# Kernel tuning notes

Measured on AMD Instinct MI355X. Metric: run time of the kernel, lower is better.

The kernel has to match this reference:

```python
import jax, jax.numpy as jnp
import numpy as np

EMBED = 1024
HEADS = 16
HEAD_DIM = EMBED // HEADS
NEG = -1e20


def setup_inputs() -> dict:
    key = jax.random.key(0)
    ks = jax.random.split(key, 12)
    N, S, E = 2, 2048, EMBED
    w = lambda k: (jax.random.normal(k, (E, E), dtype=jnp.float32) * 0.02)
    b = lambda k: (jax.random.normal(k, (E,), dtype=jnp.float32) * 0.02)
    return {
        "values": jax.random.normal(ks[0], (N, S, E), dtype=jnp.float32),
        "keys": jax.random.normal(ks[1], (N, S, E), dtype=jnp.float32),
        "query": jax.random.normal(ks[2], (N, S, E), dtype=jnp.float32),
        "mask": jnp.ones((N, S), dtype=jnp.int32),
        "Wv": w(ks[3]), "bv": b(ks[4]),
        "Wk": w(ks[5]), "bk": b(ks[6]),
        "Wq": w(ks[7]), "bq": b(ks[8]),
        "Wo": w(ks[9]), "bo": b(ks[10]),
    }


def reference(values, keys, query, mask, Wv, bv, Wk, bk, Wq, bq, Wo, bo):
    N, S, E = query.shape
    # torch nn.Linear: x @ W.T + b
    v = (values @ Wv.T + bv).reshape(N, S, HEADS, HEAD_DIM)
    k = (keys @ Wk.T + bk).reshape(N, S, HEADS, HEAD_DIM)
    q = (query @ Wq.T + bq).reshape(N, S, HEADS, HEAD_DIM)
    # full [N,H,Q,K] score matrix, as in the original einsum
    energy = jnp.einsum('nqhd,nkhd->nhqk', q, k)
    # 2D mask with mismatched dims triggers causal tril path in the original
    causal = jnp.tril(jnp.ones((S, S), dtype=bool))  # [Q,K]
    energy = jnp.where(causal[None, None, :, :], energy, NEG)
    # NOTE: original scales by sqrt(embed_size), not sqrt(head_dim)
    attn = jax.nn.softmax(energy / jnp.sqrt(jnp.float32(E)), axis=3)
    out = jnp.einsum('nhqk,nkhd->nqhd', attn, v).reshape(N, S, E)
    return out @ Wo.T + bo
```

## Files before the change

kernel.cpp:

```cpp
#include <hip/hip_runtime.h>

typedef __bf16 bf16;
typedef __bf16 bf16x8 __attribute__((ext_vector_type(8)));
typedef float floatx4 __attribute__((ext_vector_type(4)));

#define GLOAD_LDS16(gp, lp) \
  __builtin_amdgcn_global_load_lds( \
      (const __attribute__((address_space(1))) void*)(gp), \
      (__attribute__((address_space(3))) void*)(lp), 16, 0, 0)

__global__ __launch_bounds__(256) void cvt_all_kernel(
    const float* __restrict__ v, const float* __restrict__ k, const float* __restrict__ q,
    const float* __restrict__ wv, const float* __restrict__ wk,
    const float* __restrict__ wq, const float* __restrict__ wo,
    bf16* __restrict__ xv, bf16* __restrict__ xk, bf16* __restrict__ xq,
    bf16* __restrict__ bwv, bf16* __restrict__ bwk, bf16* __restrict__ bwq,
    bf16* __restrict__ bwo) {
  const int i = blockIdx.x * 256 + threadIdx.x;
  const int A4 = 1 << 20;
  const float* src; bf16* dst; int off;
  if (i < A4)            { src = v; dst = xv; off = i; }
  else if (i < 2 * A4)   { src = k; dst = xk; off = i - A4; }
  else if (i < 3 * A4)   { src = q; dst = xq; off = i - 2 * A4; }
  else {
    int j = i - 3 * A4; int r = j >> 18; off = j & ((1 << 18) - 1);
    src = (r == 0) ? wv : (r == 1) ? wk : (r == 2) ? wq : wo;
    dst = (r == 0) ? bwv : (r == 1) ? bwk : (r == 2) ? bwq : bwo;
  }
  float4 x = reinterpret_cast<const float4*>(src)[off];
  union { bf16 b[4]; short4 s; } u;
  u.b[0] = (bf16)x.x; u.b[1] = (bf16)x.y; u.b[2] = (bf16)x.z; u.b[3] = (bf16)x.w;
  reinterpret_cast<short4*>(dst)[off] = u.s;
}

template <bool OUTF32>
__device__ __forceinline__ void gemm_body(
    const bf16* __restrict__ A, const bf16* __restrict__ B,
    const float* __restrict__ bias, void* __restrict__ Cout) {
  constexpr int K = 1024, N = 1024;
  __shared__ __align__(16) bf16 As[128 * 32];
  __shared__ __align__(16) bf16 Bs[128 * 32];
  const int tid = threadIdx.x;
  const int lane = tid & 63;
  const int wave = tid >> 6;
  const int quad = lane >> 4;
  const int l16 = lane & 15;
  const int wm = (wave >> 1) * 64;
  const int wn = (wave & 1) * 64;
  const int am0 = blockIdx.y * 128;
  const int bn0 = blockIdx.x * 128;
  const int srow = lane >> 2;
  const int scol = (lane & 3) * 8;

  floatx4 acc[4][4] = {};

  for (int k0 = 0; k0 < K; k0 += 32) {
    __syncthreads();
#pragma unroll
    for (int j = 0; j < 2; j++) {
      const int chunk = wave * 2 + j;
      const int row = chunk * 16 + srow;
      GLOAD_LDS16(A + (size_t)(am0 + row) * K + k0 + scol, As + chunk * 512);
      GLOAD_LDS16(B + (size_t)(bn0 + row) * K + k0 + scol, Bs + chunk * 512);
    }
    __syncthreads();

    bf16x8 af[4], bfv[4];
#pragma unroll
    for (int mi = 0; mi < 4; mi++)
      af[mi] = *reinterpret_cast<const bf16x8*>(&As[(wm + mi * 16 + l16) * 32 + quad * 8]);
#pragma unroll
    for (int ni = 0; ni < 4; ni++)
      bfv[ni] = *reinterpret_cast<const bf16x8*>(&Bs[(wn + ni * 16 + l16) * 32 + quad * 8]);
#pragma unroll
    for (int mi = 0; mi < 4; mi++)
#pragma unroll
      for (int ni = 0; ni < 4; ni++)
        acc[mi][ni] = __builtin_amdgcn_mfma_f32_16x16x32_bf16(af[mi], bfv[ni], acc[mi][ni], 0, 0, 0);
  }

#pragma unroll
  for (int mi = 0; mi < 4; mi++) {
#pragma unroll
    for (int ni = 0; ni < 4; ni++) {
      const int col = bn0 + wn + ni * 16 + l16;
      const float bb = bias[col];
      const int row = am0 + wm + mi * 16 + quad * 4;
#pragma unroll
      for (int r = 0; r < 4; r++) {
        const float vv = acc[mi][ni][r] + bb;
        if constexpr (OUTF32)
          reinterpret_cast<float*>(Cout)[(size_t)(row + r) * N + col] = vv;
        else
          reinterpret_cast<bf16*>(Cout)[(size_t)(row + r) * N + col] = (bf16)vv;
      }
    }
  }
}

__global__ __launch_bounds__(256) void gemm_qkv(
    const bf16* __restrict__ A0, const bf16* __restrict__ B0, const float* __restrict__ c0, bf16* __restrict__ C0,
    const bf16* __restrict__ A1, const bf16* __restrict__ B1, const float* __restrict__ c1, bf16* __restrict__ C1,
    const bf16* __restrict__ A2, const bf16* __restrict__ B2, const float* __restrict__ c2, bf16* __restrict__ C2) {
  const bf16 *A, *B; const float* bias; bf16* C;
  if (blockIdx.z == 0)      { A = A0; B = B0; bias = c0; C = C0; }
  else if (blockIdx.z == 1) { A = A1; B = B1; bias = c1; C = C1; }
  else                      { A = A2; B = B2; bias = c2; C = C2; }
  gemm_body<false>(A, B, bias, C);
}

__global__ __launch_bounds__(256) void gemm_out(
    const bf16* __restrict__ A, const bf16* __restrict__ B,
    const float* __restrict__ bias, float* __restrict__ C) {
  gemm_body<true>(A, B, bias, C);
}

__global__ __launch_bounds__(256) void vtrans_kernel(
    const bf16* __restrict__ Vp, bf16* __restrict__ Vt) {
  __shared__ __align__(16) bf16 T[64 * 72];
  const int st = blockIdx.x;
  const int nh = blockIdx.y;
  const int n = nh >> 4, h = nh & 15;
  const int tid = threadIdx.x;
  {
    int c = tid;
#pragma unroll
    for (int it = 0; it < 2; it++, c += 256) {
      int r = c >> 3, col = (c & 7) * 8;
      *reinterpret_cast<int4*>(&T[r * 72 + col]) =
          *reinterpret_cast<const int4*>(Vp + ((size_t)(n * 2048 + st * 64 + r)) * 1024 + h * 64 + col);
    }
  }
  __syncthreads();
  {
    int c = tid;
#pragma unroll
    for (int it = 0; it < 2; it++, c += 256) {
      int d = c >> 3, sc = (c & 7) * 8;
      union { bf16 b[8]; int4 v; } tmp;
#pragma unroll
      for (int j = 0; j < 8; j++) tmp.b[j] = T[(sc + j) * 72 + d];
      *reinterpret_cast<int4*>(Vt + ((size_t)(nh * 64 + d)) * 2048 + st * 64 + sc) = tmp.v;
    }
  }
}

#define S_LEN 2048
#define EMB 1024
#define QT 128
#define KTILE 64
#define PSTR 72
#define SCALE2 (0.03125f * 1.44269504f)

__global__ __launch_bounds__(256) void attn_kernel(
    const bf16* __restrict__ Q, const bf16* __restrict__ K,
    const bf16* __restrict__ Vt, bf16* __restrict__ O) {
  __shared__ __align__(16) bf16 Ps[QT * PSTR];

  const int tid = threadIdx.x;
  const int lane = tid & 63;
  const int wave = tid >> 6;
  const int quad = lane >> 4;
  const int l16 = lane & 15;
  const int wq = wave * 32;

  const int id = blockIdx.x;
  const int p = id & 255;
  const int half = id >> 8;
  const int qtl = p & 7;
  const int qt = half ? (15 - qtl) : qtl;
  const int nh = p >> 3;
  const int n = nh >> 4;
  const int h = nh & 15;
  const int q0 = qt * QT;

  bf16x8 aq[2][2];
  {
    const bf16* Qb = Q + ((size_t)(n * S_LEN + q0 + wq + l16)) * EMB + h * 64 + quad * 8;
#pragma unroll
    for (int mi = 0; mi < 2; mi++)
#pragma unroll
      for (int kc = 0; kc < 2; kc++)
        aq[mi][kc] = *reinterpret_cast<const bf16x8*>(Qb + mi * 16 * EMB + kc * 32);
  }

  float l_part[2][4] = {};
  floatx4 o_acc[2][4] = {};

  const bf16* Kb = K + ((size_t)(n * S_LEN + l16)) * EMB + h * 64 + quad * 8;
  const bf16* Vb = Vt + (size_t)(nh * 64 + l16) * S_LEN + quad * 8;

  const int ktiles = 2 * qt + 2;
  for (int kt = 0; kt < ktiles; kt++) {
    const int k0 = kt * KTILE;

    floatx4 s_acc[2][4] = {};
#pragma unroll
    for (int kc = 0; kc < 2; kc++) {
      bf16x8 bk[4];
#pragma unroll
      for (int ni = 0; ni < 4; ni++)
        bk[ni] = *reinterpret_cast<const bf16x8*>(Kb + (size_t)(k0 + ni * 16) * EMB + kc * 32);
#pragma unroll
      for (int mi = 0; mi < 2; mi++)
#pragma unroll
        for (int ni = 0; ni < 4; ni++)
          s_acc[mi][ni] = __builtin_amdgcn_mfma_f32_16x16x32_bf16(aq[mi][kc], bk[ni], s_acc[mi][ni], 0, 0, 0);
    }

    const bool needMask = (k0 + KTILE - 1) > (q0 + wq);
#pragma unroll
    for (int mi = 0; mi < 2; mi++) {
#pragma unroll
      for (int ni = 0; ni < 4; ni++) {
        const int cg = k0 + ni * 16 + l16;
#pragma unroll
        for (int r = 0; r < 4; r++) {
          const int rg = q0 + wq + mi * 16 + quad * 4 + r;
          float pr = __builtin_amdgcn_exp2f(s_acc[mi][ni][r] * SCALE2);
          if (needMask) pr = (cg <= rg) ? pr : 0.f;
          s_acc[mi][ni][r] = pr;
          l_part[mi][r] += pr;
        }
      }
    }

#pragma unroll
    for (int mi = 0; mi < 2; mi++) {
#pragma unroll
      for (int ni = 0; ni < 4; ni++) {
        const int cl = ni * 2 + (l16 >> 3);
        const int pc = (cl ^ quad) * 8 + (l16 & 7);
#pragma unroll
        for (int r = 0; r < 4; r++)
          Ps[(wq + mi * 16 + quad * 4 + r) * PSTR + pc] = (bf16)s_acc[mi][ni][r];
      }
    }

#pragma unroll
    for (int kc = 0; kc < 2; kc++) {
      bf16x8 ap[2], bv[4];
      const int pc = ((kc * 4 + quad) ^ (l16 >> 2)) * 8;
#pragma unroll
      for (int mi = 0; mi < 2; mi++)
        ap[mi] = *reinterpret_cast<const bf16x8*>(&Ps[(wq + mi * 16 + l16) * PSTR + pc]);
#pragma unroll
      for (int di = 0; di < 4; di++)
        bv[di] = *reinterpret_cast<const bf16x8*>(Vb + (size_t)(di * 16) * S_LEN + k0 + kc * 32);
#pragma unroll
      for (int mi = 0; mi < 2; mi++)
#pragma unroll
        for (int di = 0; di < 4; di++)
          o_acc[mi][di] = __builtin_amdgcn_mfma_f32_16x16x32_bf16(ap[mi], bv[di], o_acc[mi][di], 0, 0, 0);
    }
  }

#pragma unroll
  for (int mi = 0; mi < 2; mi++)
#pragma unroll
    for (int r = 0; r < 4; r++) {
      float s = l_part[mi][r];
#pragma unroll
      for (int off = 1; off < 16; off <<= 1) s += __shfl_xor(s, off);
      l_part[mi][r] = 1.0f / s;
    }

  bf16* Op = O + ((size_t)(n * S_LEN + q0 + wq)) * EMB + h * 64;
#pragma unroll
  for (int mi = 0; mi < 2; mi++) {
#pragma unroll
    for (int r = 0; r < 4; r++) {
      const float inv = l_part[mi][r];
      bf16* orow = Op + (size_t)(mi * 16 + quad * 4 + r) * EMB;
#pragma unroll
      for (int di = 0; di < 4; di++)
        orow[di * 16 + l16] = (bf16)(o_acc[mi][di][r] * inv);
    }
  }
}

extern "C" void kernel_launch(void* const* d_in, const int* in_sizes, int n_in,
                              void* d_out, int out_size, void* d_ws, size_t ws_size,
                              hipStream_t stream) {
  (void)in_sizes; (void)n_in; (void)out_size; (void)ws_size;
  const float* values = (const float*)d_in[0];
  const float* keys   = (const float*)d_in[1];
  const float* query  = (const float*)d_in[2];
  const float* Wv = (const float*)d_in[4];
  const float* bv = (const float*)d_in[5];
  const float* Wk = (const float*)d_in[6];
  const float* bk = (const float*)d_in[7];
  const float* Wq = (const float*)d_in[8];
  const float* bq = (const float*)d_in[9];
  const float* Wo = (const float*)d_in[10];
  const float* bo = (const float*)d_in[11];
  float* out = (float*)d_out;

  const int NB = 2, S = 2048, E = 1024;
  const int M = NB * S;
  const size_t MB_ = 1u << 20;
  char* ws = (char*)d_ws;
  bf16* xv  = (bf16*)(ws + 0 * MB_);
  bf16* xk  = (bf16*)(ws + 8 * MB_);
  bf16* xq  = (bf16*)(ws + 16 * MB_);
  bf16* wvb = (bf16*)(ws + 24 * MB_);
  bf16* wkb = (bf16*)(ws + 26 * MB_);
  bf16* wqb = (bf16*)(ws + 28 * MB_);
  bf16* wob = (bf16*)(ws + 30 * MB_);
  bf16* vp  = (bf16*)(ws + 32 * MB_);
  bf16* kp  = (bf16*)(ws + 40 * MB_);
  bf16* qp  = (bf16*)(ws + 48 * MB_);
  bf16* ao  = (bf16*)(ws + 56 * MB_);
  bf16* vt  = (bf16*)(ws + 0 * MB_);

  cvt_all_kernel<<<(4 << 20) / 256, 256, 0, stream>>>(
      values, keys, query, Wv, Wk, Wq, Wo,
      xv, xk, xq, wvb, wkb, wqb, wob);

  gemm_qkv<<<dim3(E / 128, M / 128, 3), 256, 0, stream>>>(
      xq, wqb, bq, qp,
      xk, wkb, bk, kp,
      xv, wvb, bv, vp);

  vtrans_kernel<<<dim3(S / 64, NB * 16), 256, 0, stream>>>(vp, vt);

  attn_kernel<<<dim3(512), 256, 0, stream>>>(qp, kp, vt, ao);

  gemm_out<<<dim3(E / 128, M / 128), 256, 0, stream>>>(ao, wob, bo, out);
}
```

Measured before the change: 273.1 us.

## Write head-major Q/K and transposed V from QKV GEMM; prefetch K/V in attention

The QKV GEMM epilogue now writes Q and K in a head-major [n*h, S, 64] layout and V directly transposed to [n*h, 64, S], which removes the separate V transpose kernel and its launch and memory round trip. The attention kernel reads the contiguous per-head layout and software-pipelines the next K tile into registers while the current one is used, loading V earlier in each step. The trade-offs are more scattered epilogue stores (2-byte strided writes for Q/K, 8-byte writes for V) and higher register pressure from the double-buffered K fragments.

```diff
diff --git a/kernel.cpp b/kernel.cpp
--- a/kernel.cpp
+++ b/kernel.cpp
@@ -1,6 +1,7 @@
 #include <hip/hip_runtime.h>
 
 typedef __bf16 bf16;
+typedef __bf16 bf16x4 __attribute__((ext_vector_type(4)));
 typedef __bf16 bf16x8 __attribute__((ext_vector_type(8)));
 typedef float floatx4 __attribute__((ext_vector_type(4)));
 
@@ -33,7 +34,7 @@
   reinterpret_cast<short4*>(dst)[off] = u.s;
 }
 
-template <bool OUTF32>
+template <int MODE>
 __device__ __forceinline__ void gemm_body(
     const bf16* __restrict__ A, const bf16* __restrict__ B,
     const float* __restrict__ bias, void* __restrict__ Cout) {
@@ -86,13 +87,27 @@
       const int col = bn0 + wn + ni * 16 + l16;
       const float bb = bias[col];
       const int row = am0 + wm + mi * 16 + quad * 4;
-#pragma unroll
-      for (int r = 0; r < 4; r++) {
-        const float vv = acc[mi][ni][r] + bb;
-        if constexpr (OUTF32)
-          reinterpret_cast<float*>(Cout)[(size_t)(row + r) * N + col] = vv;
-        else
-          reinterpret_cast<bf16*>(Cout)[(size_t)(row + r) * N + col] = (bf16)vv;
+      if constexpr (MODE == 2) {
+#pragma unroll
+        for (int r = 0; r < 4; r++)
+          reinterpret_cast<float*>(Cout)[(size_t)(row + r) * N + col] = acc[mi][ni][r] + bb;
+      } else {
+        const int nb = row >> 11;
+        const int s = row & 2047;
+        const int h = col >> 6;
+        const int d = col & 63;
+        const int nh = nb * 16 + h;
+        if constexpr (MODE == 0) {
+          bf16* base = reinterpret_cast<bf16*>(Cout) + ((size_t)nh * 2048 + s) * 64 + d;
+#pragma unroll
+          for (int r = 0; r < 4; r++) base[(size_t)r * 64] = (bf16)(acc[mi][ni][r] + bb);
+        } else {
+          bf16x4 pk;
+#pragma unroll
+          for (int r = 0; r < 4; r++) pk[r] = (bf16)(acc[mi][ni][r] + bb);
+          *reinterpret_cast<bf16x4*>(
+              reinterpret_cast<bf16*>(Cout) + ((size_t)nh * 64 + d) * 2048 + s) = pk;
+        }
       }
     }
   }
@@ -102,47 +117,15 @@
     const bf16* __restrict__ A0, const bf16* __restrict__ B0, const float* __restrict__ c0, bf16* __restrict__ C0,
     const bf16* __restrict__ A1, const bf16* __restrict__ B1, const float* __restrict__ c1, bf16* __restrict__ C1,
     const bf16* __restrict__ A2, const bf16* __restrict__ B2, const float* __restrict__ c2, bf16* __restrict__ C2) {
-  const bf16 *A, *B; const float* bias; bf16* C;
-  if (blockIdx.z == 0)      { A = A0; B = B0; bias = c0; C = C0; }
-  else if (blockIdx.z == 1) { A = A1; B = B1; bias = c1; C = C1; }
-  else                      { A = A2; B = B2; bias = c2; C = C2; }
-  gemm_body<false>(A, B, bias, C);
+  if (blockIdx.z == 0)      gemm_body<0>(A0, B0, c0, C0);
+  else if (blockIdx.z == 1) gemm_body<0>(A1, B1, c1, C1);
+  else                      gemm_body<1>(A2, B2, c2, C2);
 }
 
 __global__ __launch_bounds__(256) void gemm_out(
     const bf16* __restrict__ A, const bf16* __restrict__ B,
     const float* __restrict__ bias, float* __restrict__ C) {
-  gemm_body<true>(A, B, bias, C);
-}
-
-__global__ __launch_bounds__(256) void vtrans_kernel(
-    const bf16* __restrict__ Vp, bf16* __restrict__ Vt) {
-  __shared__ __align__(16) bf16 T[64 * 72];
-  const int st = blockIdx.x;
-  const int nh = blockIdx.y;
-  const int n = nh >> 4, h = nh & 15;
-  const int tid = threadIdx.x;
-  {
-    int c = tid;
-#pragma unroll
-    for (int it = 0; it < 2; it++, c += 256) {
-      int r = c >> 3, col = (c & 7) * 8;
-      *reinterpret_cast<int4*>(&T[r * 72 + col]) =
-          *reinterpret_cast<const int4*>(Vp + ((size_t)(n * 2048 + st * 64 + r)) * 1024 + h * 64 + col);
-    }
-  }
-  __syncthreads();
-  {
-    int c = tid;
-#pragma unroll
-    for (int it = 0; it < 2; it++, c += 256) {
-      int d = c >> 3, sc = (c & 7) * 8;
-      union { bf16 b[8]; int4 v; } tmp;
-#pragma unroll
-      for (int j = 0; j < 8; j++) tmp.b[j] = T[(sc + j) * 72 + d];
-      *reinterpret_cast<int4*>(Vt + ((size_t)(nh * 64 + d)) * 2048 + st * 64 + sc) = tmp.v;
-    }
-  }
+  gemm_body<2>(A, B, bias, C);
 }
 
 #define S_LEN 2048
@@ -153,7 +136,7 @@
 #define SCALE2 (0.03125f * 1.44269504f)
 
 __global__ __launch_bounds__(256) void attn_kernel(
-    const bf16* __restrict__ Q, const bf16* __restrict__ K,
+    const bf16* __restrict__ Qh, const bf16* __restrict__ Kh,
     const bf16* __restrict__ Vt, bf16* __restrict__ O) {
   __shared__ __align__(16) bf16 Ps[QT * PSTR];
 
@@ -176,37 +159,49 @@
 
   bf16x8 aq[2][2];
   {
-    const bf16* Qb = Q + ((size_t)(n * S_LEN + q0 + wq + l16)) * EMB + h * 64 + quad * 8;
+    const bf16* Qb = Qh + ((size_t)nh * S_LEN + q0 + wq + l16) * 64 + quad * 8;
 #pragma unroll
     for (int mi = 0; mi < 2; mi++)
 #pragma unroll
       for (int kc = 0; kc < 2; kc++)
-        aq[mi][kc] = *reinterpret_cast<const bf16x8*>(Qb + mi * 16 * EMB + kc * 32);
+        aq[mi][kc] = *reinterpret_cast<const bf16x8*>(Qb + mi * 16 * 64 + kc * 32);
   }
 
   float l_part[2][4] = {};
   floatx4 o_acc[2][4] = {};
 
-  const bf16* Kb = K + ((size_t)(n * S_LEN + l16)) * EMB + h * 64 + quad * 8;
-  const bf16* Vb = Vt + (size_t)(nh * 64 + l16) * S_LEN + quad * 8;
-
-  const int ktiles = 2 * qt + 2;
-  for (int kt = 0; kt < ktiles; kt++) {
-    const int k0 = kt * KTILE;
+  const bf16* Kb = Kh + ((size_t)nh * S_LEN + l16) * 64 + quad * 8;
+  const bf16* Vb = Vt + ((size_t)nh * 64 + l16) * S_LEN + quad * 8;
+
+  bf16x8 kb[2][2][4];
+
+#pragma unroll
+  for (int kc = 0; kc < 2; kc++)
+#pragma unroll
+    for (int ni = 0; ni < 4; ni++)
+      kb[0][kc][ni] = *reinterpret_cast<const bf16x8*>(Kb + (size_t)(ni * 16) * 64 + kc * 32);
+
+  auto step = [&](int k0, bf16x8 (&kcur)[2][4], bf16x8 (&knx)[2][4], int k0n) {
+    bf16x8 vb[2][4];
+#pragma unroll
+    for (int kc = 0; kc < 2; kc++)
+#pragma unroll
+      for (int di = 0; di < 4; di++)
+        vb[kc][di] = *reinterpret_cast<const bf16x8*>(Vb + (size_t)(di * 16) * S_LEN + k0 + kc * 32);
+#pragma unroll
+    for (int kc = 0; kc < 2; kc++)
+#pragma unroll
+      for (int ni = 0; ni < 4; ni++)
+        knx[kc][ni] = *reinterpret_cast<const bf16x8*>(Kb + (size_t)(k0n + ni * 16) * 64 + kc * 32);
 
     floatx4 s_acc[2][4] = {};
 #pragma unroll
-    for (int kc = 0; kc < 2; kc++) {
-      bf16x8 bk[4];
-#pragma unroll
-      for (int ni = 0; ni < 4; ni++)
-        bk[ni] = *reinterpret_cast<const bf16x8*>(Kb + (size_t)(k0 + ni * 16) * EMB + kc * 32);
+    for (int kc = 0; kc < 2; kc++)
 #pragma unroll
       for (int mi = 0; mi < 2; mi++)
 #pragma unroll
         for (int ni = 0; ni < 4; ni++)
-          s_acc[mi][ni] = __builtin_amdgcn_mfma_f32_16x16x32_bf16(aq[mi][kc], bk[ni], s_acc[mi][ni], 0, 0, 0);
-    }
+          s_acc[mi][ni] = __builtin_amdgcn_mfma_f32_16x16x32_bf16(aq[mi][kc], kcur[kc][ni], s_acc[mi][ni], 0, 0, 0);
 
     const bool needMask = (k0 + KTILE - 1) > (q0 + wq);
 #pragma unroll
@@ -239,20 +234,26 @@
 
 #pragma unroll
     for (int kc = 0; kc < 2; kc++) {
-      bf16x8 ap[2], bv[4];
+      bf16x8 ap[2];
       const int pc = ((kc * 4 + quad) ^ (l16 >> 2)) * 8;
 #pragma unroll
       for (int mi = 0; mi < 2; mi++)
         ap[mi] = *reinterpret_cast<const bf16x8*>(&Ps[(wq + mi * 16 + l16) * PSTR + pc]);
 #pragma unroll
-      for (int di = 0; di < 4; di++)
-        bv[di] = *reinterpret_cast<const bf16x8*>(Vb + (size_t)(di * 16) * S_LEN + k0 + kc * 32);
-#pragma unroll
       for (int mi = 0; mi < 2; mi++)
 #pragma unroll
         for (int di = 0; di < 4; di++)
-          o_acc[mi][di] = __builtin_amdgcn_mfma_f32_16x16x32_bf16(ap[mi], bv[di], o_acc[mi][di], 0, 0, 0);
-    }
+          o_acc[mi][di] = __builtin_amdgcn_mfma_f32_16x16x32_bf16(ap[mi], vb[kc][di], o_acc[mi][di], 0, 0, 0);
+    }
+  };
+
+  const int ktiles = 2 * qt + 2;
+  for (int kt = 0; kt < ktiles; kt += 2) {
+    const int k0a = kt * KTILE;
+    const int k0b = k0a + KTILE;
+    const int k0c = (kt + 2 < ktiles) ? (kt + 2) * KTILE : 0;
+    step(k0a, kb[0], kb[1], k0b);
+    step(k0b, kb[1], kb[0], k0c);
   }
 
 #pragma unroll
@@ -307,24 +308,21 @@
   bf16* wkb = (bf16*)(ws + 26 * MB_);
   bf16* wqb = (bf16*)(ws + 28 * MB_);
   bf16* wob = (bf16*)(ws + 30 * MB_);
-  bf16* vp  = (bf16*)(ws + 32 * MB_);
-  bf16* kp  = (bf16*)(ws + 40 * MB_);
-  bf16* qp  = (bf16*)(ws + 48 * MB_);
+  bf16* kh  = (bf16*)(ws + 32 * MB_);
+  bf16* qh  = (bf16*)(ws + 40 * MB_);
+  bf16* vt  = (bf16*)(ws + 48 * MB_);
   bf16* ao  = (bf16*)(ws + 56 * MB_);
-  bf16* vt  = (bf16*)(ws + 0 * MB_);
 
   cvt_all_kernel<<<(4 << 20) / 256, 256, 0, stream>>>(
       values, keys, query, Wv, Wk, Wq, Wo,
       xv, xk, xq, wvb, wkb, wqb, wob);
 
   gemm_qkv<<<dim3(E / 128, M / 128, 3), 256, 0, stream>>>(
-      xq, wqb, bq, qp,
-      xk, wkb, bk, kp,
-      xv, wvb, bv, vp);
-
-  vtrans_kernel<<<dim3(S / 64, NB * 16), 256, 0, stream>>>(vp, vt);
-
-  attn_kernel<<<dim3(512), 256, 0, stream>>>(qp, kp, vt, ao);
+      xq, wqb, bq, qh,
+      xk, wkb, bk, kh,
+      xv, wvb, bv, vt);
+
+  attn_kernel<<<dim3(512), 256, 0, stream>>>(qh, kh, vt, ao);
 
   gemm_out<<<dim3(E / 128, M / 128), 256, 0, stream>>>(ao, wob, bo, out);
 }
```

Result: faster. 254.9 us (-6.6%).
